# Kernel tuning notes

Measured on AMD Instinct MI355X. Metric: run time of the kernel, lower is better.

Reference implementation:

```python
import jax, jax.numpy as jnp
import numpy as np

B, S, H = 32, 2048, 1024


def setup_inputs() -> dict:
    key = jax.random.key(0)
    ks = jax.random.split(key, 7)
    return {
        "query": jax.random.normal(ks[0], (B, 1, H), dtype=jnp.float32),
        "key": jax.random.normal(ks[1], (S, B, H), dtype=jnp.float32),
        "Wa_w": jax.random.normal(ks[2], (H, H), dtype=jnp.float32) / np.sqrt(H),
        "Wa_b": jax.random.normal(ks[3], (H,), dtype=jnp.float32) * 0.01,
        "Ua_w": jax.random.normal(ks[4], (H, H), dtype=jnp.float32) / np.sqrt(H),
        "Ua_b": jax.random.normal(ks[5], (H,), dtype=jnp.float32) * 0.01,
        "va_w": jax.random.normal(ks[6], (H,), dtype=jnp.float32) / np.sqrt(H),
        "va_b": jnp.zeros((1,), dtype=jnp.float32),
    }


def reference(query, key, Wa_w, Wa_b, Ua_w, Ua_b, va_w, va_b):
    # key: (S, B, H) -> (B, S, H)
    k = jnp.transpose(key, (1, 0, 2))
    # additive (Bahdanau) energies: tanh(Wa q + Ua k), broadcast over S
    e = jnp.tanh((query @ Wa_w + Wa_b) + (k @ Ua_w + Ua_b))  # (B, S, H)
    scores = jnp.einsum("bsh,h->bs", e, va_w) + va_b[0]       # (B, S)
    weights = jax.nn.softmax(scores, axis=-1)[:, None, :]      # (B, 1, S)
    context = jnp.einsum("bqs,bsh->bqh", weights, k)           # (B, 1, H)
    return context, weights
```

## Files before the change

### kernel.cpp

```cpp
#include <hip/hip_runtime.h>

#define Hdim 1024
#define Bdim 32
#define Sdim 2048

typedef __attribute__((ext_vector_type(8))) __bf16 bf16x8;
typedef __attribute__((ext_vector_type(4))) float f32x4;

#define GLOAD_LDS16(gp, lp)                                                              \
  __builtin_amdgcn_global_load_lds(                                                     \
      (const __attribute__((address_space(1))) unsigned int*)(gp),                      \
      (__attribute__((address_space(3))) unsigned int*)(lp), 16, 0, 0)

__global__ __launch_bounds__(256) void convert_ua_kernel(const float* __restrict__ Ua,
                                                         __bf16* __restrict__ ubt) {
  int du = blockIdx.x * 256 + threadIdx.x;
  int n  = du & 127;
  int k8 = (du >> 7) & 127;
  int nt = du >> 14;
  int ng = nt * 128 + n;
  bf16x8 t;
#pragma unroll
  for (int j = 0; j < 8; ++j)
    t[j] = (__bf16)Ua[(k8 * 8 + j) * Hdim + ng];
  *(bf16x8*)(ubt + (size_t)du * 8) = t;
}

__global__ __launch_bounds__(256) void qc_kernel(const float* __restrict__ q,
                                                 const float* __restrict__ Wa,
                                                 const float* __restrict__ Wab,
                                                 const float* __restrict__ Uab,
                                                 float* __restrict__ qc) {
  int b = blockIdx.y;
  int h = blockIdx.x * 256 + threadIdx.x;
  float acc = Wab[h] + Uab[h];
  const float* qr = q + b * Hdim;
#pragma unroll 16
  for (int i = 0; i < Hdim; ++i)
    acc = fmaf(qr[i], Wa[i * Hdim + h], acc);
  qc[b * Hdim + h] = acc;
}

__global__ __launch_bounds__(256) void gemm_scores_kernel(const float* __restrict__ key,
                                                          const __bf16* __restrict__ ubt,
                                                          const float* __restrict__ qc,
                                                          const float* __restrict__ va,
                                                          float* __restrict__ part) {
  __shared__ __align__(16) float AsQ[4096];
  __shared__ __align__(16) __bf16 Bs[4096];
  __shared__ float red[256];

  const int tid  = threadIdx.x;
  const int w    = tid >> 6;
  const int lane = tid & 63;
  const int quad = lane >> 4;
  const int l16  = lane & 15;
  const int nt = blockIdx.x;
  const int mt = blockIdx.y;
  const int r0 = mt * 128;
  const int n0 = nt * 128;
  const int wm = (w & 1) * 64;
  const int wn = (w >> 1) * 64;

  f32x4 acc[4][4] = {};

  for (int kc = 0; kc < Hdim; kc += 32) {
#pragma unroll
    for (int it = 0; it < 4; ++it) {
      int u  = it * 256 + tid;
      int k4 = u >> 7, row = u & 127;
      GLOAD_LDS16(key + (size_t)(r0 + row) * Hdim + kc + k4 * 4, AsQ + u * 4);
    }
#pragma unroll
    for (int it = 0; it < 2; ++it) {
      int u = it * 256 + tid;
      GLOAD_LDS16(ubt + ((size_t)nt * 16384 + (kc >> 3) * 128 + u) * 8, Bs + u * 8);
    }
    __syncthreads();

    bf16x8 bfr[4];
#pragma unroll
    for (int j = 0; j < 4; ++j)
      bfr[j] = *(const bf16x8*)&Bs[(quad * 128 + wn + j * 16 + l16) * 8];

    bf16x8 afr[4];
#pragma unroll
    for (int i = 0; i < 4; ++i) {
      int ml = wm + i * 16 + l16;
      float4 f0 = *(const float4*)&AsQ[((quad * 2) * 128 + ml) * 4];
      float4 f1 = *(const float4*)&AsQ[((quad * 2 + 1) * 128 + ml) * 4];
      bf16x8 a;
      a[0] = (__bf16)f0.x; a[1] = (__bf16)f0.y; a[2] = (__bf16)f0.z; a[3] = (__bf16)f0.w;
      a[4] = (__bf16)f1.x; a[5] = (__bf16)f1.y; a[6] = (__bf16)f1.z; a[7] = (__bf16)f1.w;
      afr[i] = a;
    }

#pragma unroll
    for (int i = 0; i < 4; ++i)
#pragma unroll
      for (int j = 0; j < 4; ++j)
        acc[i][j] = __builtin_amdgcn_mfma_f32_16x16x32_bf16(afr[i], bfr[j], acc[i][j], 0, 0, 0);

    __syncthreads();
  }

#pragma unroll
  for (int it = 0; it < 16; ++it) {
    int u = it * 256 + tid;
    AsQ[u] = qc[(u >> 7) * Hdim + n0 + (u & 127)];
  }
  __syncthreads();

  float vav[4];
#pragma unroll
  for (int j = 0; j < 4; ++j) vav[j] = va[n0 + wn + j * 16 + l16];

#pragma unroll
  for (int i = 0; i < 4; ++i) {
#pragma unroll
    for (int rg = 0; rg < 4; ++rg) {
      int b = (i & 1) * 16 + quad * 4 + rg;
      float sum = 0.f;
#pragma unroll
      for (int j = 0; j < 4; ++j) {
        float v = acc[i][j][rg] + AsQ[b * 128 + wn + j * 16 + l16];
        v = fminf(fmaxf(v, -15.f), 15.f);
        float e = __expf(2.f * v);
        sum += (e - 1.f) * __builtin_amdgcn_rcpf(e + 1.f) * vav[j];
      }
#pragma unroll
      for (int off = 1; off < 16; off <<= 1)
        sum += __shfl_xor(sum, off, 64);
      if (l16 == 0)
        red[(wm + i * 16 + quad * 4 + rg) * 2 + (w >> 1)] = sum;
    }
  }
  __syncthreads();
  if (tid < 128)
    part[(size_t)(r0 + tid) * 8 + nt] = red[tid * 2] + red[tid * 2 + 1];
}

__global__ __launch_bounds__(256) void softmax_kernel(const float* __restrict__ part,
                                                      float* __restrict__ dout) {
  int b = blockIdx.x, t = threadIdx.x;
  int w = t >> 6, lane = t & 63;
  __shared__ float red1[4], red2[4];
  float sc[8];
  float m = -1e30f;
#pragma unroll
  for (int c = 0; c < 8; ++c) {
    int s = c * 256 + t;
    const float4* p = (const float4*)&part[(size_t)(s * 32 + b) * 8];
    float4 p0 = p[0], p1 = p[1];
    float v = ((p0.x + p0.y) + (p0.z + p0.w)) + ((p1.x + p1.y) + (p1.z + p1.w));
    sc[c] = v;
    m = fmaxf(m, v);
  }
#pragma unroll
  for (int off = 1; off < 64; off <<= 1) m = fmaxf(m, __shfl_xor(m, off, 64));
  if (lane == 0) red1[w] = m;
  __syncthreads();
  m = fmaxf(fmaxf(red1[0], red1[1]), fmaxf(red1[2], red1[3]));
  float sum = 0.f;
#pragma unroll
  for (int c = 0; c < 8; ++c) { sc[c] = __expf(sc[c] - m); sum += sc[c]; }
#pragma unroll
  for (int off = 1; off < 64; off <<= 1) sum += __shfl_xor(sum, off, 64);
  if (lane == 0) red2[w] = sum;
  __syncthreads();
  float inv = 1.f / (red2[0] + red2[1] + red2[2] + red2[3]);
#pragma unroll
  for (int c = 0; c < 8; ++c)
    dout[32768 + b * 2048 + c * 256 + t] = sc[c] * inv;
}

__global__ __launch_bounds__(256) void ctx_part_kernel(const float* __restrict__ key,
                                                       const float* __restrict__ dout,
                                                       float* __restrict__ cpart) {
  int sc = blockIdx.x;
  int b  = blockIdx.y;
  int t  = threadIdx.x;
  float4 acc = make_float4(0.f, 0.f, 0.f, 0.f);
  int s0 = sc * 64;
#pragma unroll 8
  for (int s = s0; s < s0 + 64; ++s) {
    float wgt = dout[32768 + b * 2048 + s];
    float4 k4 = *(const float4*)&key[((size_t)(s * 32 + b) << 10) + t * 4];
    acc.x = fmaf(wgt, k4.x, acc.x);
    acc.y = fmaf(wgt, k4.y, acc.y);
    acc.z = fmaf(wgt, k4.z, acc.z);
    acc.w = fmaf(wgt, k4.w, acc.w);
  }
  *(float4*)&cpart[((size_t)(sc * 32 + b) << 10) + t * 4] = acc;
}

__global__ __launch_bounds__(256) void ctx_reduce_kernel(const float* __restrict__ cpart,
                                                         float* __restrict__ dout) {
  int o = blockIdx.x * 256 + threadIdx.x;
  int b = o >> 10, h = o & 1023;
  float s = 0.f;
#pragma unroll
  for (int sc = 0; sc < 32; ++sc)
    s += cpart[((size_t)(sc * 32 + b) << 10) + h];
  dout[o] = s;
}

extern "C" void kernel_launch(void* const* d_in, const int* in_sizes, int n_in,
                              void* d_out, int out_size, void* d_ws, size_t ws_size,
                              hipStream_t stream) {
  const float* q   = (const float*)d_in[0];
  const float* key = (const float*)d_in[1];
  const float* Waw = (const float*)d_in[2];
  const float* Wab = (const float*)d_in[3];
  const float* Uaw = (const float*)d_in[4];
  const float* Uab = (const float*)d_in[5];
  const float* vaw = (const float*)d_in[6];
  float* out = (float*)d_out;

  char* ws = (char*)d_ws;
  float*  qc    = (float*)(ws);
  __bf16* ubt   = (__bf16*)(ws + (131072));
  float*  part  = (float*)(ws + (131072 + 2097152));
  float*  cpart = (float*)(ws + (131072 + 2097152 + 2097152));

  convert_ua_kernel<<<512, 256, 0, stream>>>(Uaw, ubt);
  qc_kernel<<<dim3(4, 32), 256, 0, stream>>>(q, Waw, Wab, Uab, qc);
  gemm_scores_kernel<<<dim3(8, 512), 256, 0, stream>>>(key, ubt, qc, vaw, part);
  softmax_kernel<<<32, 256, 0, stream>>>(part, out);
  ctx_part_kernel<<<dim3(32, 32), 256, 0, stream>>>(key, out, cpart);
  ctx_reduce_kernel<<<128, 256, 0, stream>>>(cpart, out);
}
```

Baseline: 808.7 us.

## Pre-convert key to bf16 and remap GEMM blocks for XCD-local L2 reuse

Adds a pass that converts the fp32 key tensor to bf16 in workspace, and a scores GEMM variant that streams bf16 key tiles straight into LDS instead of loading fp32 and converting there. Both the new and the old GEMM now use a 1-D grid remapped so the 8 column tiles of one row tile land on the same XCD in sequence. That should let L2 serve the repeated key reads. The conversion adds a full extra read and write of key, plus a large workspace requirement; if the workspace is too small, the code falls back to the fp32 path.

```diff
diff --git a/kernel.cpp b/kernel.cpp
--- a/kernel.cpp
+++ b/kernel.cpp
@@ -11,6 +11,17 @@
   __builtin_amdgcn_global_load_lds(                                                     \
       (const __attribute__((address_space(1))) unsigned int*)(gp),                      \
       (__attribute__((address_space(3))) unsigned int*)(lp), 16, 0, 0)
+
+__global__ __launch_bounds__(256) void convert_key_kernel(const float* __restrict__ key,
+                                                          __bf16* __restrict__ bkey) {
+  size_t idx = (size_t)blockIdx.x * 256 + threadIdx.x;
+  const float4* src = (const float4*)(key + idx * 8);
+  float4 f0 = src[0], f1 = src[1];
+  bf16x8 t;
+  t[0] = (__bf16)f0.x; t[1] = (__bf16)f0.y; t[2] = (__bf16)f0.z; t[3] = (__bf16)f0.w;
+  t[4] = (__bf16)f1.x; t[5] = (__bf16)f1.y; t[6] = (__bf16)f1.z; t[7] = (__bf16)f1.w;
+  *(bf16x8*)(bkey + idx * 8) = t;
+}
 
 __global__ __launch_bounds__(256) void convert_ua_kernel(const float* __restrict__ Ua,
                                                          __bf16* __restrict__ ubt) {
@@ -41,6 +52,104 @@
   qc[b * Hdim + h] = acc;
 }
 
+__global__ __launch_bounds__(256) void gemm_scores_bf16_kernel(const __bf16* __restrict__ bkey,
+                                                               const __bf16* __restrict__ ubt,
+                                                               const float* __restrict__ qc,
+                                                               const float* __restrict__ va,
+                                                               float* __restrict__ part) {
+  __shared__ __align__(16) __bf16 ABs[8192];
+  __shared__ float red[256];
+
+  const int tid  = threadIdx.x;
+  const int w    = tid >> 6;
+  const int lane = tid & 63;
+  const int quad = lane >> 4;
+  const int l16  = lane & 15;
+
+  const int l   = blockIdx.x;
+  const int xcd = l & 7;
+  const int i2  = l >> 3;
+  const int mt  = xcd * 64 + (i2 >> 3);
+  const int nt  = i2 & 7;
+
+  const int r0 = mt * 128;
+  const int n0 = nt * 128;
+  const int wm = (w & 1) * 64;
+  const int wn = (w >> 1) * 64;
+
+  __bf16* As = ABs;
+  __bf16* Bs = ABs + 4096;
+
+  f32x4 acc[4][4] = {};
+
+  for (int kc = 0; kc < Hdim; kc += 32) {
+#pragma unroll
+    for (int it = 0; it < 2; ++it) {
+      int u  = it * 256 + tid;
+      int k8 = u >> 7, row = u & 127;
+      GLOAD_LDS16(bkey + (size_t)(r0 + row) * Hdim + kc + k8 * 8, As + u * 8);
+    }
+#pragma unroll
+    for (int it = 0; it < 2; ++it) {
+      int u = it * 256 + tid;
+      GLOAD_LDS16(ubt + ((size_t)nt * 16384 + (kc >> 3) * 128 + u) * 8, Bs + u * 8);
+    }
+    __syncthreads();
+
+    bf16x8 afr[4], bfr[4];
+#pragma unroll
+    for (int i = 0; i < 4; ++i)
+      afr[i] = *(const bf16x8*)&As[(quad * 128 + wm + i * 16 + l16) * 8];
+#pragma unroll
+    for (int j = 0; j < 4; ++j)
+      bfr[j] = *(const bf16x8*)&Bs[(quad * 128 + wn + j * 16 + l16) * 8];
+
+#pragma unroll
+    for (int i = 0; i < 4; ++i)
+#pragma unroll
+      for (int j = 0; j < 4; ++j)
+        acc[i][j] = __builtin_amdgcn_mfma_f32_16x16x32_bf16(afr[i], bfr[j], acc[i][j], 0, 0, 0);
+
+    __syncthreads();
+  }
+
+  float* qcs = (float*)ABs;
+#pragma unroll
+  for (int it = 0; it < 16; ++it) {
+    int u = it * 256 + tid;
+    qcs[u] = qc[(u >> 7) * Hdim + n0 + (u & 127)];
+  }
+  __syncthreads();
+
+  float vav[4];
+#pragma unroll
+  for (int j = 0; j < 4; ++j) vav[j] = va[n0 + wn + j * 16 + l16];
+
+#pragma unroll
+  for (int i = 0; i < 4; ++i) {
+#pragma unroll
+    for (int rg = 0; rg < 4; ++rg) {
+      int b = (i & 1) * 16 + quad * 4 + rg;
+      float sum = 0.f;
+#pragma unroll
+      for (int j = 0; j < 4; ++j) {
+        float v = acc[i][j][rg] + qcs[b * 128 + wn + j * 16 + l16];
+        v = fminf(fmaxf(v, -15.f), 15.f);
+        float e = __expf(2.f * v);
+        sum += (e - 1.f) * __builtin_amdgcn_rcpf(e + 1.f) * vav[j];
+      }
+#pragma unroll
+      for (int off = 1; off < 16; off <<= 1)
+        sum += __shfl_xor(sum, off, 64);
+      if (l16 == 0)
+        red[(wm + i * 16 + quad * 4 + rg) * 2 + (w >> 1)] = sum;
+    }
+  }
+  __syncthreads();
+  if (tid < 128)
+    part[(size_t)(r0 + tid) * 8 + nt] = red[tid * 2] + red[tid * 2 + 1];
+}
+
 __global__ __launch_bounds__(256) void gemm_scores_kernel(const float* __restrict__ key,
                                                           const __bf16* __restrict__ ubt,
                                                           const float* __restrict__ qc,
@@ -55,8 +164,11 @@
   const int lane = tid & 63;
   const int quad = lane >> 4;
   const int l16  = lane & 15;
-  const int nt = blockIdx.x;
-  const int mt = blockIdx.y;
+  const int l   = blockIdx.x;
+  const int xcd = l & 7;
+  const int i2  = l >> 3;
+  const int mt  = xcd * 64 + (i2 >> 3);
+  const int nt  = i2 & 7;
   const int r0 = mt * 128;
   const int n0 = nt * 128;
   const int wm = (w & 1) * 64;
@@ -219,13 +331,20 @@
 
   char* ws = (char*)d_ws;
   float*  qc    = (float*)(ws);
-  __bf16* ubt   = (__bf16*)(ws + (131072));
-  float*  part  = (float*)(ws + (131072 + 2097152));
-  float*  cpart = (float*)(ws + (131072 + 2097152 + 2097152));
+  __bf16* ubt   = (__bf16*)(ws + 131072);
+  float*  part  = (float*)(ws + 131072 + 2097152);
+  float*  cpart = (float*)(ws + 131072 + 2097152 + 2097152);
+  __bf16* bkey  = (__bf16*)(ws + 131072 + 2097152 + 2097152 + 4194304);
+  const size_t need = 131072ull + 2097152 + 2097152 + 4194304 + 134217728;
 
   convert_ua_kernel<<<512, 256, 0, stream>>>(Uaw, ubt);
   qc_kernel<<<dim3(4, 32), 256, 0, stream>>>(q, Waw, Wab, Uab, qc);
-  gemm_scores_kernel<<<dim3(8, 512), 256, 0, stream>>>(key, ubt, qc, vaw, part);
+  if (ws_size >= need) {
+    convert_key_kernel<<<32768, 256, 0, stream>>>(key, bkey);
+    gemm_scores_bf16_kernel<<<4096, 256, 0, stream>>>(bkey, ubt, qc, vaw, part);
+  } else {
+    gemm_scores_kernel<<<4096, 256, 0, stream>>>(key, ubt, qc, vaw, part);
+  }
   softmax_kernel<<<32, 256, 0, stream>>>(part, out);
   ctx_part_kernel<<<dim3(32, 32), 256, 0, stream>>>(key, out, cpart);
   ctx_reduce_kernel<<<128, 256, 0, stream>>>(cpart, out);
```

After: 716.0 us. -11.5%, faster.
